# Kernel optimization log

Hardware: AMD Instinct MI355X
Metric: run time of the kernel (lower is better)

## Reference

```python
import jax, jax.numpy as jnp
import numpy as np

B, T = 64, 2000
Q_DIM, MEM_DIM = 1024, 512
ATTN_DIM, N_FILTERS, KERNEL = 128, 32, 31


def setup_inputs() -> dict:
    key = jax.random.key(0)
    ks = jax.random.split(key, 8)
    s = lambda fan_in: 1.0 / np.sqrt(fan_in)
    return {
        "query": jax.random.normal(ks[0], (B, Q_DIM), jnp.float32),
        "memory": jax.random.normal(ks[1], (B, T, MEM_DIM), jnp.float32),
        "attention_weights_cat": jax.random.uniform(ks[2], (B, 2, T), jnp.float32),
        "Wq": jax.random.normal(ks[3], (Q_DIM, ATTN_DIM), jnp.float32) * s(Q_DIM),
        "Wm": jax.random.normal(ks[4], (MEM_DIM, ATTN_DIM), jnp.float32) * s(MEM_DIM),
        "conv_kernel": jax.random.normal(ks[5], (KERNEL, 2, N_FILTERS), jnp.float32) * s(KERNEL * 2),
        "Wloc": jax.random.normal(ks[6], (N_FILTERS, ATTN_DIM), jnp.float32) * s(N_FILTERS),
        "V": jax.random.normal(ks[7], (ATTN_DIM,), jnp.float32) * s(ATTN_DIM),
    }


def reference(query, memory, attention_weights_cat, Wq, Wm, conv_kernel, Wloc, V):
    # processed_query: [B, 1, A] (tanh-activated Dense, no bias)
    pq = jnp.tanh(query @ Wq)[:, None, :]
    # processed_memory: [B, T, A]
    pm = jnp.tanh(jnp.einsum('btd,da->bta', memory, Wm))
    # location features: [B, 2, T] -> [B, T, 2] -> Conv1D(same) -> [B, T, F]
    awc = jnp.transpose(attention_weights_cat, (0, 2, 1))
    conv = jax.lax.conv_general_dilated(
        awc, conv_kernel, window_strides=(1,), padding='SAME',
        dimension_numbers=('NWC', 'WIO', 'NWC'))
    ploc = jnp.tanh(jnp.einsum('btf,fa->bta', conv, Wloc))
    # energies: [B, T]
    energies = jnp.einsum('bta,a->bt', jnp.tanh(pq + ploc + pm), V)
    attention_weights = jax.nn.softmax(energies, axis=1)
    attention_context = jnp.einsum('bt,btd->bd', attention_weights, memory)
    return attention_context, attention_weights
```

## Files before the change

kernel.cpp:

```cpp
#include <hip/hip_runtime.h>
#include <stdint.h>

#define B_ 64
#define T_ 2000
#define QD 1024
#define MD 512
#define AD 128
#define NF 32
#define KW 31
#define TT 16
#define NCHT 125
#define NCH 5
#define GPB 25

typedef short bf16x8 __attribute__((ext_vector_type(8)));
typedef float f32x4 __attribute__((ext_vector_type(4)));

#define WAITCNT(vm, lgkm) (((vm) & 15) | (7 << 4) | (((lgkm) & 15) << 8) | (((vm) >> 4) << 14))

__device__ __forceinline__ unsigned short f2bf(float f) {
    union { float f; uint32_t u; } v; v.f = f;
    uint32_t u = v.u;
    return (unsigned short)((u + 0x7FFFu + ((u >> 16) & 1u)) >> 16);
}

__device__ __forceinline__ uint32_t pkbf(float a, float b) {
    union { float f; uint32_t u; } x, y; x.f = a; y.f = b;
    uint32_t ra = (x.u + 0x7FFFu + ((x.u >> 16) & 1u)) >> 16;
    uint32_t rb = (y.u + 0x7FFFu + ((y.u >> 16) & 1u)) & 0xFFFF0000u;
    return ra | rb;
}

__device__ __forceinline__ float fast_tanhf(float x) {
    x = fminf(15.f, fmaxf(-15.f, x));
    float e = __expf(2.f * x);
    return __fdividef(e - 1.f, e + 1.f);
}

__device__ __forceinline__ void dma16(const float* src, void* lds_dst) {
    __builtin_amdgcn_global_load_lds(
        (const __attribute__((address_space(1))) void*)src,
        (__attribute__((address_space(3))) void*)lds_dst, 16, 0, 0);
}

__device__ __forceinline__ void stage_tile(const float* __restrict__ rowbase,
                                           void* lds_base, int wave, int lane) {
    #pragma unroll
    for (int s8 = 0; s8 < 8; ++s8) {
        int seg = wave * 8 + s8;
        int row = seg >> 1;
        int gsrc = (((seg & 1) << 6) | lane) ^ row;
        dma16(rowbase + row * MD + gsrc * 4, (char*)lds_base + seg * 1024);
    }
}

__global__ __launch_bounds__(128) void prep1_kernel(
    const float* __restrict__ query, const float* __restrict__ Wq,
    const float* __restrict__ Wm, const float* __restrict__ Wloc,
    float* __restrict__ pqpart, unsigned short* __restrict__ wmp,
    unsigned short* __restrict__ wlp)
{
    int blk = blockIdx.x, tid = threadIdx.x;
    if (blk < 512) {
        int b = blk >> 3, sl = blk & 7;
        const float* qq = query + b * QD + sl * 128;
        const float* wq = Wq + (size_t)(sl * 128) * AD + tid;
        float s = 0.f;
        #pragma unroll 4
        for (int d = 0; d < 128; ++d) s += qq[d] * wq[(size_t)d * AD];
        pqpart[(b * 8 + sl) * AD + tid] = s;
    } else if (blk < 528) {
        int kt = blk - 512;
        int nt = tid >> 4, c = tid & 15;
        for (int q = 0; q < 4; ++q)
            for (int j = 0; j < 8; ++j)
                wmp[(((kt * 8 + nt) * 64) + q * 16 + c) * 8 + j] =
                    f2bf(Wm[(kt * 32 + q * 8 + j) * AD + nt * 16 + c]);
    } else {
        int nt = tid >> 4, c = tid & 15;
        for (int q = 0; q < 4; ++q)
            for (int j = 0; j < 8; ++j)
                wlp[((nt * 64) + q * 16 + c) * 8 + j] =
                    f2bf(Wloc[(q * 8 + j) * AD + nt * 16 + c]);
    }
}

__global__ __launch_bounds__(256) void conv_kernel(
    const float* __restrict__ awc, const float* __restrict__ kern,
    unsigned short* __restrict__ cfrag)
{
    const int ci = blockIdx.x, b = blockIdx.y;
    const int t0 = ci * TT;
    const int tid = threadIdx.x;
    const int f = tid & 31, tA = tid >> 5, tB = tA + 8;
    const float* a0p = awc + (b * 2 + 0) * T_;
    const float* a1p = awc + (b * 2 + 1) * T_;
    float sA = 0.f, sB = 0.f;
    #pragma unroll
    for (int k = 0; k < KW; ++k) {
        float k0 = kern[(k * 2 + 0) * NF + f];
        float k1 = kern[(k * 2 + 1) * NF + f];
        int xA = t0 + tA + k - 15, xB = t0 + tB + k - 15;
        float wA0 = (xA >= 0 && xA < T_) ? a0p[xA] : 0.f;
        float wA1 = (xA >= 0 && xA < T_) ? a1p[xA] : 0.f;
        float wB0 = (xB >= 0 && xB < T_) ? a0p[xB] : 0.f;
        float wB1 = (xB >= 0 && xB < T_) ? a1p[xB] : 0.f;
        sA = fmaf(wA0, k0, sA); sA = fmaf(wA1, k1, sA);
        sB = fmaf(wB0, k0, sB); sB = fmaf(wB1, k1, sB);
    }
    unsigned short* base = cfrag + (size_t)(b * NCHT + ci) * 64 * 8;
    base[((f >> 3) * 16 + tA) * 8 + (f & 7)] = f2bf(sA);
    base[((f >> 3) * 16 + tB) * 8 + (f & 7)] = f2bf(sB);
}

__global__ __launch_bounds__(256, 2) void energy_kernel(
    const float* __restrict__ mem, const float* __restrict__ V,
    const float* __restrict__ pqpart,
    const unsigned short* __restrict__ wmp, const unsigned short* __restrict__ wlp,
    const unsigned short* __restrict__ cfrag,
    float* __restrict__ p_ws, float* __restrict__ Lpart, float* __restrict__ ctxpart)
{
    const int g = blockIdx.x, b = blockIdx.y;
    const int tid = threadIdx.x, lane = tid & 63, wave = tid >> 6;
    const int c0 = g * NCH;
    const int q = lane >> 4, cx = lane & 15;
    const int nt0 = wave * 2;

    __shared__ __align__(16) float mem_s[2][TT][MD];
    __shared__ float epart[TT][4];
    __shared__ float pex[TT];

    const float* memb = mem + (size_t)b * T_ * MD;

    const int a0 = nt0 * 16 + cx, a1 = a0 + 16;
    float pq0a = 0.f, pq1a = 0.f;
    #pragma unroll
    for (int sl = 0; sl < 8; ++sl) {
        pq0a += pqpart[(b * 8 + sl) * AD + a0];
        pq1a += pqpart[(b * 8 + sl) * AD + a1];
    }
    const float pq0 = fast_tanhf(pq0a), pq1 = fast_tanhf(pq1a);
    const float v0 = V[a0], v1 = V[a1];
    const bf16x8 wl0 = *(const bf16x8*)(wlp + ((nt0 + 0) * 64 + lane) * 8);
    const bf16x8 wl1 = *(const bf16x8*)(wlp + ((nt0 + 1) * 64 + lane) * 8);

    const unsigned short* cfb = cfrag + ((size_t)(b * NCHT + c0) * 64 + lane) * 8;
    bf16x8 af = *(const bf16x8*)cfb;

    float ctx0 = 0.f, ctx1 = 0.f;

    stage_tile(memb + (size_t)(c0 + 0) * TT * MD, &mem_s[0][0][0], wave, lane);
    stage_tile(memb + (size_t)(c0 + 1) * TT * MD, &mem_s[1][0][0], wave, lane);

    for (int i = 0; i < NCH; ++i) {
        const int cb = i & 1;
        const int t0 = (c0 + i) * TT;

        if (i + 1 < NCH) __builtin_amdgcn_s_waitcnt(WAITCNT(8, 0));
        else             __builtin_amdgcn_s_waitcnt(WAITCNT(0, 0));
        __builtin_amdgcn_s_barrier();

        f32x4 accl0 = {}, accl1 = {}, accm0 = {}, accm1 = {};
        accl0 = __builtin_amdgcn_mfma_f32_16x16x32_bf16(af, wl0, accl0, 0, 0, 0);
        accl1 = __builtin_amdgcn_mfma_f32_16x16x32_bf16(af, wl1, accl1, 0, 0, 0);
        {
            const float* tb = &mem_s[cb][0][0];
            #pragma unroll 4
            for (int kt = 0; kt < 16; ++kt) {
                int gr0 = kt * 8 + 2 * q;
                float4 x0 = *(const float4*)(tb + (cx * 128 + ((gr0 + 0) ^ cx)) * 4);
                float4 x1 = *(const float4*)(tb + (cx * 128 + ((gr0 + 1) ^ cx)) * 4);
                union { bf16x8 v; uint32_t w[4]; } u;
                u.w[0] = pkbf(x0.x, x0.y); u.w[1] = pkbf(x0.z, x0.w);
                u.w[2] = pkbf(x1.x, x1.y); u.w[3] = pkbf(x1.z, x1.w);
                bf16x8 b0 = *(const bf16x8*)(wmp + (((kt * 8 + nt0 + 0) * 64) + lane) * 8);
                bf16x8 b1 = *(const bf16x8*)(wmp + (((kt * 8 + nt0 + 1) * 64) + lane) * 8);
                accm0 = __builtin_amdgcn_mfma_f32_16x16x32_bf16(u.v, b0, accm0, 0, 0, 0);
                accm1 = __builtin_amdgcn_mfma_f32_16x16x32_bf16(u.v, b1, accm1, 0, 0, 0);
            }
        }

        #pragma unroll
        for (int r = 0; r < 4; ++r) {
            int tl = q * 4 + r;
            float s = fast_tanhf(pq0 + fast_tanhf(accl0[r]) + fast_tanhf(accm0[r])) * v0
                    + fast_tanhf(pq1 + fast_tanhf(accl1[r]) + fast_tanhf(accm1[r])) * v1;
            s += __shfl_xor(s, 1);
            s += __shfl_xor(s, 2);
            s += __shfl_xor(s, 4);
            s += __shfl_xor(s, 8);
            if (cx == 0) epart[tl][wave] = s;
        }
        __builtin_amdgcn_s_waitcnt(WAITCNT(63, 0));
        __builtin_amdgcn_s_barrier();

        if (tid < TT) {
            float e = epart[tid][0] + epart[tid][1] + epart[tid][2] + epart[tid][3];
            float pv = __expf(e);
            pex[tid] = pv;
            p_ws[b * T_ + t0 + tid] = pv;
            float Ls = pv;
            Ls += __shfl_xor(Ls, 1);
            Ls += __shfl_xor(Ls, 2);
            Ls += __shfl_xor(Ls, 4);
            Ls += __shfl_xor(Ls, 8);
            if (tid == 0) Lpart[b * NCHT + c0 + i] = Ls;
        }
        __builtin_amdgcn_s_waitcnt(WAITCNT(63, 0));
        __builtin_amdgcn_s_barrier();

        {
            const float* tb = &mem_s[cb][0][0];
            int g0 = tid >> 2, g1 = (tid + 256) >> 2, sub = tid & 3;
            #pragma unroll
            for (int tl = 0; tl < TT; ++tl) {
                float w = pex[tl];
                ctx0 = fmaf(w, tb[(tl * 128 + (g0 ^ tl)) * 4 + sub], ctx0);
                ctx1 = fmaf(w, tb[(tl * 128 + (g1 ^ tl)) * 4 + sub], ctx1);
            }
        }
        __builtin_amdgcn_s_waitcnt(WAITCNT(63, 0));
        __builtin_amdgcn_s_barrier();

        if (i + 1 < NCH) af = *(const bf16x8*)(cfb + (size_t)(i + 1) * 64 * 8);
        if (i + 2 < NCH)
            stage_tile(memb + (size_t)(c0 + i + 2) * TT * MD, &mem_s[cb][0][0], wave, lane);
    }

    float* cp = ctxpart + (size_t)(b * GPB + g) * MD;
    cp[tid] = ctx0;
    cp[tid + 256] = ctx1;
}

__global__ __launch_bounds__(256) void finalize_kernel(
    const float* __restrict__ p_ws, const float* __restrict__ Lpart,
    const float* __restrict__ ctxpart, float* __restrict__ out)
{
    int part = blockIdx.x, b = blockIdx.y, tid = threadIdx.x;
    __shared__ float ws4[4];
    float s = (tid < NCHT) ? Lpart[b * NCHT + tid] : 0.f;
    s += __shfl_xor(s, 1);  s += __shfl_xor(s, 2);
    s += __shfl_xor(s, 4);  s += __shfl_xor(s, 8);
    s += __shfl_xor(s, 16); s += __shfl_xor(s, 32);
    if ((tid & 63) == 0) ws4[tid >> 6] = s;
    __syncthreads();
    float invL = 1.f / (ws4[0] + ws4[1] + ws4[2] + ws4[3]);
    if (part == 4) {
        float c0 = 0.f, c1 = 0.f;
        for (int gg = 0; gg < GPB; ++gg) {
            const float* cp = ctxpart + (size_t)(b * GPB + gg) * MD;
            c0 += cp[tid];
            c1 += cp[tid + 256];
        }
        out[b * MD + tid] = c0 * invL;
        out[b * MD + tid + 256] = c1 * invL;
    } else {
        int t0 = part * 500;
        for (int t = t0 + tid; t < t0 + 500; t += 256)
            out[B_ * MD + b * T_ + t] = p_ws[b * T_ + t] * invL;
    }
}

extern "C" void kernel_launch(void* const* d_in, const int* in_sizes, int n_in,
                              void* d_out, int out_size, void* d_ws, size_t ws_size,
                              hipStream_t stream) {
    const float* query  = (const float*)d_in[0];
    const float* memory = (const float*)d_in[1];
    const float* awc    = (const float*)d_in[2];
    const float* Wq     = (const float*)d_in[3];
    const float* Wm     = (const float*)d_in[4];
    const float* kern   = (const float*)d_in[5];
    const float* Wloc   = (const float*)d_in[6];
    const float* V      = (const float*)d_in[7];
    float* out = (float*)d_out;

    char* ws = (char*)d_ws;
    float*          pqpart = (float*)(ws + 0);
    unsigned short* wmp    = (unsigned short*)(ws + 262144);
    unsigned short* wlp    = (unsigned short*)(ws + 393216);
    unsigned short* cfrag  = (unsigned short*)(ws + 401408);
    float*          p_ws   = (float*)(ws + 8593408);
    float*          Lpart  = (float*)(ws + 9105408);
    float*          ctxp   = (float*)(ws + 9137408);

    prep1_kernel<<<529, 128, 0, stream>>>(query, Wq, Wm, Wloc, pqpart, wmp, wlp);
    conv_kernel<<<dim3(NCHT, B_), 256, 0, stream>>>(awc, kern, cfrag);
    energy_kernel<<<dim3(GPB, B_), 256, 0, stream>>>(
        memory, V, pqpart, wmp, wlp, cfrag, p_ws, Lpart, ctxp);
    finalize_kernel<<<dim3(5, B_), 256, 0, stream>>>(p_ws, Lpart, ctxp, out);
}
```

Baseline: 508.2 us.

## Restage memory pipeline, truncate bf16 packing, vectorize context accumulation

Replaces round-to-nearest bf16 packing of memory tiles with a single byte-permute truncation, cutting ALU work in the MFMA inner loop at some cost in rounding accuracy. The double-buffer schedule changes: the next tile and its conv fragment are issued right after the top-of-loop barrier, and the trailing barrier at the end of each iteration is removed. Context accumulation now has each thread read a float4 from one of two row halves instead of doing scalar reads, and writes twice as many partial context rows, which finalize sums. The epart reduction also uses a single float4 LDS read.

After: 499.2 us. About the same (-1.8%).

```diff
diff --git a/kernel.cpp b/kernel.cpp
--- a/kernel.cpp
+++ b/kernel.cpp
@@ -24,11 +24,9 @@
     return (unsigned short)((u + 0x7FFFu + ((u >> 16) & 1u)) >> 16);
 }
 
-__device__ __forceinline__ uint32_t pkbf(float a, float b) {
-    union { float f; uint32_t u; } x, y; x.f = a; y.f = b;
-    uint32_t ra = (x.u + 0x7FFFu + ((x.u >> 16) & 1u)) >> 16;
-    uint32_t rb = (y.u + 0x7FFFu + ((y.u >> 16) & 1u)) & 0xFFFF0000u;
-    return ra | rb;
+__device__ __forceinline__ uint32_t pktrunc(float lo, float hi) {
+    union { float f; uint32_t u; } a, c; a.f = lo; c.f = hi;
+    return __builtin_amdgcn_perm(a.u, c.u, 0x03020706u);
 }
 
 __device__ __forceinline__ float fast_tanhf(float x) {
@@ -127,7 +125,7 @@
     const int nt0 = wave * 2;
 
     __shared__ __align__(16) float mem_s[2][TT][MD];
-    __shared__ float epart[TT][4];
+    __shared__ __align__(16) float epart[TT][4];
     __shared__ float pex[TT];
 
     const float* memb = mem + (size_t)b * T_ * MD;
@@ -146,19 +144,25 @@
 
     const unsigned short* cfb = cfrag + ((size_t)(b * NCHT + c0) * 64 + lane) * 8;
     bf16x8 af = *(const bf16x8*)cfb;
-
-    float ctx0 = 0.f, ctx1 = 0.f;
+    bf16x8 af_next = af;
+
+    f32x4 ctx = {};
+    const int gq = tid & 127, h = tid >> 7;
 
     stage_tile(memb + (size_t)(c0 + 0) * TT * MD, &mem_s[0][0][0], wave, lane);
-    stage_tile(memb + (size_t)(c0 + 1) * TT * MD, &mem_s[1][0][0], wave, lane);
 
     for (int i = 0; i < NCH; ++i) {
         const int cb = i & 1;
-        const int t0 = (c0 + i) * TT;
-
-        if (i + 1 < NCH) __builtin_amdgcn_s_waitcnt(WAITCNT(8, 0));
-        else             __builtin_amdgcn_s_waitcnt(WAITCNT(0, 0));
+        const int t0c = (c0 + i) * TT;
+
+        __builtin_amdgcn_s_waitcnt(WAITCNT(0, 0));
         __builtin_amdgcn_s_barrier();
+
+        if (i + 1 < NCH) {
+            stage_tile(memb + (size_t)(c0 + i + 1) * TT * MD,
+                       &mem_s[(i + 1) & 1][0][0], wave, lane);
+            af_next = *(const bf16x8*)(cfb + (size_t)(i + 1) * 64 * 8);
+        }
 
         f32x4 accl0 = {}, accl1 = {}, accm0 = {}, accm1 = {};
         accl0 = __builtin_amdgcn_mfma_f32_16x16x32_bf16(af, wl0, accl0, 0, 0, 0);
@@ -171,8 +175,8 @@
                 float4 x0 = *(const float4*)(tb + (cx * 128 + ((gr0 + 0) ^ cx)) * 4);
                 float4 x1 = *(const float4*)(tb + (cx * 128 + ((gr0 + 1) ^ cx)) * 4);
                 union { bf16x8 v; uint32_t w[4]; } u;
-                u.w[0] = pkbf(x0.x, x0.y); u.w[1] = pkbf(x0.z, x0.w);
-                u.w[2] = pkbf(x1.x, x1.y); u.w[3] = pkbf(x1.z, x1.w);
+                u.w[0] = pktrunc(x0.x, x0.y); u.w[1] = pktrunc(x0.z, x0.w);
+                u.w[2] = pktrunc(x1.x, x1.y); u.w[3] = pktrunc(x1.z, x1.w);
                 bf16x8 b0 = *(const bf16x8*)(wmp + (((kt * 8 + nt0 + 0) * 64) + lane) * 8);
                 bf16x8 b1 = *(const bf16x8*)(wmp + (((kt * 8 + nt0 + 1) * 64) + lane) * 8);
                 accm0 = __builtin_amdgcn_mfma_f32_16x16x32_bf16(u.v, b0, accm0, 0, 0, 0);
@@ -195,10 +199,10 @@
         __builtin_amdgcn_s_barrier();
 
         if (tid < TT) {
-            float e = epart[tid][0] + epart[tid][1] + epart[tid][2] + epart[tid][3];
-            float pv = __expf(e);
+            float4 ep = *(const float4*)&epart[tid][0];
+            float pv = __expf(ep.x + ep.y + ep.z + ep.w);
             pex[tid] = pv;
-            p_ws[b * T_ + t0 + tid] = pv;
+            p_ws[b * T_ + t0c + tid] = pv;
             float Ls = pv;
             Ls += __shfl_xor(Ls, 1);
             Ls += __shfl_xor(Ls, 2);
@@ -211,25 +215,22 @@
 
         {
             const float* tb = &mem_s[cb][0][0];
-            int g0 = tid >> 2, g1 = (tid + 256) >> 2, sub = tid & 3;
             #pragma unroll
-            for (int tl = 0; tl < TT; ++tl) {
-                float w = pex[tl];
-                ctx0 = fmaf(w, tb[(tl * 128 + (g0 ^ tl)) * 4 + sub], ctx0);
-                ctx1 = fmaf(w, tb[(tl * 128 + (g1 ^ tl)) * 4 + sub], ctx1);
+            for (int r = 0; r < 8; ++r) {
+                int row = r * 2 + h;
+                float w = pex[row];
+                float4 m4 = *(const float4*)(tb + (row * 128 + (gq ^ row)) * 4);
+                ctx.x = fmaf(w, m4.x, ctx.x);
+                ctx.y = fmaf(w, m4.y, ctx.y);
+                ctx.z = fmaf(w, m4.z, ctx.z);
+                ctx.w = fmaf(w, m4.w, ctx.w);
             }
         }
-        __builtin_amdgcn_s_waitcnt(WAITCNT(63, 0));
-        __builtin_amdgcn_s_barrier();
-
-        if (i + 1 < NCH) af = *(const bf16x8*)(cfb + (size_t)(i + 1) * 64 * 8);
-        if (i + 2 < NCH)
-            stage_tile(memb + (size_t)(c0 + i + 2) * TT * MD, &mem_s[cb][0][0], wave, lane);
-    }
-
-    float* cp = ctxpart + (size_t)(b * GPB + g) * MD;
-    cp[tid] = ctx0;
-    cp[tid + 256] = ctx1;
+        af = af_next;
+    }
+
+    float* cp = ctxpart + ((size_t)((b * GPB + g) * 2 + h)) * MD + gq * 4;
+    *(float4*)cp = *(float4*)&ctx;
 }
 
 __global__ __launch_bounds__(256) void finalize_kernel(
@@ -247,8 +248,9 @@
     float invL = 1.f / (ws4[0] + ws4[1] + ws4[2] + ws4[3]);
     if (part == 4) {
         float c0 = 0.f, c1 = 0.f;
-        for (int gg = 0; gg < GPB; ++gg) {
-            const float* cp = ctxpart + (size_t)(b * GPB + gg) * MD;
+        const float* cpb = ctxpart + (size_t)(b * GPB * 2) * MD;
+        for (int gg = 0; gg < GPB * 2; ++gg) {
+            const float* cp = cpb + (size_t)gg * MD;
             c0 += cp[tid];
             c1 += cp[tid + 256];
         }
```
